# Kernel tuning notes

Measured on AMD Instinct MI355X. Metric: run time of the kernel, lower is better.

## Reference

```python
import jax, jax.numpy as jnp
import numpy as np

EMBED_DIM = 768
N_HEADS = 12
HEAD_DIM = EMBED_DIM // N_HEADS
B, T = 2, 4096


def setup_inputs() -> dict:
    key = jax.random.key(0)
    k1, k2, k3, k4, k5 = jax.random.split(key, 5)
    s = 1.0 / np.sqrt(EMBED_DIM)
    return {
        "x": jax.random.normal(k1, (B, T, EMBED_DIM), dtype=jnp.float32),
        "Wqkv": jax.random.normal(k2, (EMBED_DIM, 3 * EMBED_DIM), dtype=jnp.float32) * s,
        "bqkv": jnp.zeros((3 * EMBED_DIM,), dtype=jnp.float32),
        "Wproj": jax.random.normal(k3, (EMBED_DIM, EMBED_DIM), dtype=jnp.float32) * s,
        "bproj": jnp.zeros((EMBED_DIM,), dtype=jnp.float32),
    }


def reference(x, Wqkv, bqkv, Wproj, bproj):
    Bz, Tz, C = x.shape
    qkv = x @ Wqkv + bqkv                         # [B,T,3C]
    q, k, v = jnp.split(qkv, 3, axis=2)
    # [B,T,H,D] -> [B,H,T,D]
    def heads(t):
        return t.reshape(Bz, Tz, N_HEADS, HEAD_DIM).transpose(0, 2, 1, 3)
    q, k, v = heads(q), heads(k), heads(v)
    scale = 1.0 / np.sqrt(HEAD_DIM)
    att = jnp.einsum("bhqd,bhkd->bhqk", q, k) * scale   # [B,H,T,T]
    causal = jnp.tril(jnp.ones((Tz, Tz), dtype=bool))
    att = jnp.where(causal[None, None], att, -jnp.inf)
    att = jax.nn.softmax(att, axis=-1)
    y = jnp.einsum("bhqk,bhkd->bhqd", att, v)            # [B,H,T,D]
    y = y.transpose(0, 2, 1, 3).reshape(Bz, Tz, C)
    return y @ Wproj + bproj
```

## Files before the change

kernel.cpp:

```cpp
#include <hip/hip_runtime.h>
#include <math.h>
#include <stdint.h>

typedef __attribute__((ext_vector_type(8))) short bf16x8;
typedef __attribute__((ext_vector_type(4))) float f32x4;

__device__ __forceinline__ unsigned short f2bf(float f) {
    union { float f; unsigned u; } v; v.f = f;
    return (unsigned short)((v.u + 0x7fffu + ((v.u >> 16) & 1u)) >> 16);
}

__device__ __forceinline__ void gld_lds16(const void* g, void* l) {
    __builtin_amdgcn_global_load_lds(
        (const __attribute__((address_space(1))) unsigned*)(uintptr_t)g,
        (__attribute__((address_space(3))) unsigned*)(uintptr_t)l, 16, 0, 0);
}

__global__ void k_convert(const float* __restrict__ in, unsigned short* __restrict__ out, int n4) {
    int i = blockIdx.x * blockDim.x + threadIdx.x;
    if (i >= n4) return;
    float4 f = ((const float4*)in)[i];
    ushort4 o;
    o.x = f2bf(f.x); o.y = f2bf(f.y); o.z = f2bf(f.z); o.w = f2bf(f.w);
    ((ushort4*)out)[i] = o;
}

__global__ void k_transpose(const float* __restrict__ in, unsigned short* __restrict__ out, int R, int C) {
    __shared__ float tile[32][33];
    int c0 = blockIdx.x * 32, r0 = blockIdx.y * 32;
    int tx = threadIdx.x, ty = threadIdx.y;
#pragma unroll
    for (int i = 0; i < 4; ++i)
        tile[ty + i * 8][tx] = in[(size_t)(r0 + ty + i * 8) * C + c0 + tx];
    __syncthreads();
#pragma unroll
    for (int i = 0; i < 4; ++i)
        out[(size_t)(c0 + ty + i * 8) * R + r0 + tx] = f2bf(tile[tx][ty + i * 8]);
}

#define LDT 32

__device__ __forceinline__ void gemm_core(
    const unsigned short* __restrict__ A, const unsigned short* __restrict__ Bt,
    int K, unsigned short* As, unsigned short* Bs, f32x4 (&acc)[4][4])
{
    const int tid  = threadIdx.x;
    const int lane = tid & 63;
    const int w    = tid >> 6;
    const int wm   = (w >> 1) * 64, wn = (w & 1) * 64;
    const int l15  = lane & 15, quad = lane >> 4;
    const int m0 = blockIdx.x * 128, n0 = blockIdx.y * 128;

    const f32x4 zero = {0.f, 0.f, 0.f, 0.f};
#pragma unroll
    for (int i = 0; i < 4; ++i)
#pragma unroll
        for (int j = 0; j < 4; ++j) acc[i][j] = zero;

    const int r0 = tid >> 2, p8 = (tid & 3) * 8;
    const unsigned short* Ag0 = A  + (size_t)(m0 + r0) * K + p8;
    const unsigned short* Ag1 = A  + (size_t)(m0 + r0 + 64) * K + p8;
    const unsigned short* Bg0 = Bt + (size_t)(n0 + r0) * K + p8;
    const unsigned short* Bg1 = Bt + (size_t)(n0 + r0 + 64) * K + p8;
    unsigned short* lA0 = As + r0 * LDT + p8;
    unsigned short* lA1 = lA0 + 64 * LDT;
    unsigned short* lB0 = Bs + r0 * LDT + p8;
    unsigned short* lB1 = lB0 + 64 * LDT;

    const int nk = K >> 5;
    for (int kt = 0; kt < nk; ++kt) {
        __syncthreads();
        gld_lds16(Ag0, lA0);
        gld_lds16(Ag1, lA1);
        gld_lds16(Bg0, lB0);
        gld_lds16(Bg1, lB1);
        Ag0 += 32; Ag1 += 32; Bg0 += 32; Bg1 += 32;
        __syncthreads();
        bf16x8 af[4], bfr[4];
#pragma unroll
        for (int mi = 0; mi < 4; ++mi)
            af[mi] = *(const bf16x8*)&As[(wm + mi * 16 + l15) * LDT + quad * 8];
#pragma unroll
        for (int nj = 0; nj < 4; ++nj)
            bfr[nj] = *(const bf16x8*)&Bs[(wn + nj * 16 + l15) * LDT + quad * 8];
#pragma unroll
        for (int mi = 0; mi < 4; ++mi)
#pragma unroll
            for (int nj = 0; nj < 4; ++nj)
                acc[mi][nj] = __builtin_amdgcn_mfma_f32_16x16x32_bf16(af[mi], bfr[nj], acc[mi][nj], 0, 0, 0);
    }
}

__global__ __launch_bounds__(256) void k_gemm_qkv(
    const unsigned short* __restrict__ A, const unsigned short* __restrict__ Bt,
    const float* __restrict__ bias,
    unsigned short* __restrict__ QL, unsigned short* __restrict__ KL,
    unsigned short* __restrict__ VL)
{
    __shared__ __align__(16) unsigned short As[128 * LDT];
    __shared__ __align__(16) unsigned short Bs[128 * LDT];
    f32x4 acc[4][4];
    gemm_core(A, Bt, 768, As, Bs, acc);

    const int tid = threadIdx.x, lane = tid & 63, w = tid >> 6;
    const int wm = (w >> 1) * 64, wn = (w & 1) * 64;
    const int l15 = lane & 15, quad = lane >> 4;
    const int m0 = blockIdx.x * 128, n0 = blockIdx.y * 128;
    const float cscale = 0.18033688011f;
#pragma unroll
    for (int nj = 0; nj < 4; ++nj) {
        int cg = n0 + wn + nj * 16 + l15;
        float bv = bias[cg];
        int which = cg / 768;
        int rem = cg - which * 768;
        int hd = rem >> 6, d = rem & 63;
        float sc = (which == 0) ? cscale : 1.0f;
#pragma unroll
        for (int mi = 0; mi < 4; ++mi) {
#pragma unroll
            for (int r = 0; r < 4; ++r) {
                int rg = m0 + wm + mi * 16 + quad * 4 + r;
                int b = rg >> 12, tk = rg & 4095;
                int bh = b * 12 + hd;
                unsigned short ob = f2bf((acc[mi][nj][r] + bv) * sc);
                if (which == 0) {
                    size_t idx = ((((size_t)bh * 128 + (tk >> 5)) * 2 + ((tk >> 4) & 1)) * 2 + (d >> 5)) * 512
                               + ((d >> 3) & 3) * 128 + (tk & 15) * 8 + (d & 7);
                    QL[idx] = ob;
                } else if (which == 1) {
                    size_t idx = ((((size_t)bh * 64 + (tk >> 6)) * 4 + ((tk >> 4) & 3)) * 2 + (d >> 5)) * 512
                               + ((d >> 3) & 3) * 128 + (tk & 15) * 8 + (d & 7);
                    KL[idx] = ob;
                } else {
                    int wi = tk & 63;
                    size_t idx = ((((size_t)bh * 64 + (tk >> 6)) * 4 + (d >> 4)) * 2 + (wi >> 5)) * 512
                               + ((wi >> 3) & 3) * 128 + (d & 15) * 8 + (wi & 7);
                    VL[idx] = ob;
                }
            }
        }
    }
}

__global__ __launch_bounds__(256) void k_gemm_proj(
    const unsigned short* __restrict__ A, const unsigned short* __restrict__ Bt,
    const float* __restrict__ bias, float* __restrict__ out)
{
    __shared__ __align__(16) unsigned short As[128 * LDT];
    __shared__ __align__(16) unsigned short Bs[128 * LDT];
    f32x4 acc[4][4];
    gemm_core(A, Bt, 768, As, Bs, acc);

    const int tid = threadIdx.x, lane = tid & 63, w = tid >> 6;
    const int wm = (w >> 1) * 64, wn = (w & 1) * 64;
    const int l15 = lane & 15, quad = lane >> 4;
    const int m0 = blockIdx.x * 128, n0 = blockIdx.y * 128;
#pragma unroll
    for (int nj = 0; nj < 4; ++nj) {
        int cg = n0 + wn + nj * 16 + l15;
        float bv = bias[cg];
#pragma unroll
        for (int mi = 0; mi < 4; ++mi)
#pragma unroll
            for (int r = 0; r < 4; ++r) {
                int rg = m0 + wm + mi * 16 + quad * 4 + r;
                out[(size_t)rg * 768 + cg] = acc[mi][nj][r] + bv;
            }
    }
}

#define LDP 68

__global__ __launch_bounds__(256) void k_attn(
    const unsigned short* __restrict__ QL, const unsigned short* __restrict__ KL,
    const unsigned short* __restrict__ VL, unsigned short* __restrict__ Y)
{
    __shared__ __align__(16) char smem[34816];
    unsigned short* Ps = (unsigned short*)smem;
    float* Cb = (float*)smem;

    const int tid = threadIdx.x, lane = tid & 63;
    const int w = __builtin_amdgcn_readfirstlane(tid >> 6);
    const int l15 = lane & 15, quad = lane >> 4;
    const int id = blockIdx.x;
    const int bh = id % 24;
    const int qi = 127 - id / 24;
    const int q0 = qi * 32;
    const int nkt = qi / 2 + 1;
    const int lo = (nkt * w) >> 2, hi = (nkt * (w + 1)) >> 2;
    unsigned short* Pw = Ps + w * 2 * 32 * LDP;

    const int pw_off = l15 * LDP + quad * 4;
    const int pr_off = l15 * LDP + quad * 8;

    const unsigned short* Qb = QL + (((size_t)bh * 128 + qi) * 4) * 512 + lane * 8;
    const unsigned short* kp = KL + ((size_t)bh * 64 + lo) * 4096 + lane * 8;
    const unsigned short* vp = VL + ((size_t)bh * 64 + lo) * 4096 + lane * 8;

    bf16x8 qt[2][2];
#pragma unroll
    for (int m = 0; m < 2; ++m)
#pragma unroll
        for (int h = 0; h < 2; ++h)
            qt[m][h] = *(const bf16x8*)(Qb + (m * 2 + h) * 512);

    const f32x4 zero = {0.f, 0.f, 0.f, 0.f};
    f32x4 O[2][4], lac[2];
#pragma unroll
    for (int m = 0; m < 2; ++m) {
        lac[m] = zero;
#pragma unroll
        for (int dj = 0; dj < 4; ++dj) O[m][dj] = zero;
    }

    const short ONE = (short)0x3F80;
    const bf16x8 onesf = {ONE, ONE, ONE, ONE, ONE, ONE, ONE, ONE};

    if (lo < hi) {
        bf16x8 ka[4][2], vf[4][2];
#pragma unroll
        for (int i = 0; i < 4; ++i)
#pragma unroll
            for (int h = 0; h < 2; ++h)
                ka[i][h] = *(const bf16x8*)(kp + (i * 2 + h) * 512);
#pragma unroll
        for (int dj = 0; dj < 4; ++dj)
#pragma unroll
            for (int h = 0; h < 2; ++h)
                vf[dj][h] = *(const bf16x8*)(vp + (dj * 2 + h) * 512);

        {
            f32x4 st[2][4];
#pragma unroll
            for (int i = 0; i < 4; ++i)
#pragma unroll
                for (int m = 0; m < 2; ++m) {
                    f32x4 z = __builtin_amdgcn_mfma_f32_16x16x32_bf16(ka[i][0], qt[m][0], zero, 0, 0, 0);
                    st[m][i] = __builtin_amdgcn_mfma_f32_16x16x32_bf16(ka[i][1], qt[m][1], z, 0, 0, 0);
                }
            if (lo == nkt - 1) {
                const int kb = lo * 64;
#pragma unroll
                for (int m = 0; m < 2; ++m)
#pragma unroll
                    for (int i = 0; i < 4; ++i)
#pragma unroll
                        for (int r = 0; r < 4; ++r)
                            if (kb + i * 16 + quad * 4 + r > q0 + m * 16 + l15)
                                st[m][i][r] = -INFINITY;
            }
#pragma unroll
            for (int m = 0; m < 2; ++m)
#pragma unroll
                for (int i = 0; i < 4; ++i) {
                    unsigned e0 = __float_as_uint(__builtin_amdgcn_exp2f(st[m][i][0])) + 0x8000u;
                    unsigned e1 = __float_as_uint(__builtin_amdgcn_exp2f(st[m][i][1])) + 0x8000u;
                    unsigned e2 = __float_as_uint(__builtin_amdgcn_exp2f(st[m][i][2])) + 0x8000u;
                    unsigned e3 = __float_as_uint(__builtin_amdgcn_exp2f(st[m][i][3])) + 0x8000u;
                    uint2 pk;
                    pk.x = __builtin_amdgcn_perm(e1, e0, 0x07060302);
                    pk.y = __builtin_amdgcn_perm(e3, e2, 0x07060302);
                    *(uint2*)(Pw + pw_off + m * 16 * LDP + i * 16) = pk;
                }
        }

        for (int kt = lo; kt < hi; ++kt) {
            unsigned short* bc = Pw + ((kt - lo) & 1) * 32 * LDP;
            unsigned short* bn = Pw + (((kt - lo) & 1) ^ 1) * 32 * LDP;
            const bool more = (kt + 1 < hi);

            bf16x8 pa[2][2];
#pragma unroll
            for (int m = 0; m < 2; ++m) {
                pa[m][0] = *(const bf16x8*)(bc + pr_off + m * 16 * LDP);
                pa[m][1] = *(const bf16x8*)(bc + pr_off + m * 16 * LDP + 32);
            }

            if (more) {
                kp += 4096;
#pragma unroll
                for (int i = 0; i < 4; ++i)
#pragma unroll
                    for (int h = 0; h < 2; ++h)
                        ka[i][h] = *(const bf16x8*)(kp + (i * 2 + h) * 512);
            }

#pragma unroll
            for (int m = 0; m < 2; ++m) {
                f32x4 z = __builtin_amdgcn_mfma_f32_16x16x32_bf16(pa[m][0], onesf, lac[m], 0, 0, 0);
                lac[m] = __builtin_amdgcn_mfma_f32_16x16x32_bf16(pa[m][1], onesf, z, 0, 0, 0);
            }
#pragma unroll
            for (int dj = 0; dj < 4; ++dj)
#pragma unroll
                for (int m = 0; m < 2; ++m) {
                    f32x4 z = __builtin_amdgcn_mfma_f32_16x16x32_bf16(pa[m][0], vf[dj][0], O[m][dj], 0, 0, 0);
                    O[m][dj] = __builtin_amdgcn_mfma_f32_16x16x32_bf16(pa[m][1], vf[dj][1], z, 0, 0, 0);
                }

            if (more) {
                vp += 4096;
#pragma unroll
                for (int dj = 0; dj < 4; ++dj)
#pragma unroll
                    for (int h = 0; h < 2; ++h)
                        vf[dj][h] = *(const bf16x8*)(vp + (dj * 2 + h) * 512);

                f32x4 st[2][4];
#pragma unroll
                for (int i = 0; i < 4; ++i)
#pragma unroll
                    for (int m = 0; m < 2; ++m) {
                        f32x4 z = __builtin_amdgcn_mfma_f32_16x16x32_bf16(ka[i][0], qt[m][0], zero, 0, 0, 0);
                        st[m][i] = __builtin_amdgcn_mfma_f32_16x16x32_bf16(ka[i][1], qt[m][1], z, 0, 0, 0);
                    }
                if (kt + 1 == nkt - 1) {
                    const int kb = (kt + 1) * 64;
#pragma unroll
                    for (int m = 0; m < 2; ++m)
#pragma unroll
                        for (int i = 0; i < 4; ++i)
#pragma unroll
                            for (int r = 0; r < 4; ++r)
                                if (kb + i * 16 + quad * 4 + r > q0 + m * 16 + l15)
                                    st[m][i][r] = -INFINITY;
                }
#pragma unroll
                for (int m = 0; m < 2; ++m)
#pragma unroll
                    for (int i = 0; i < 4; ++i) {
                        unsigned e0 = __float_as_uint(__builtin_amdgcn_exp2f(st[m][i][0])) + 0x8000u;
                        unsigned e1 = __float_as_uint(__builtin_amdgcn_exp2f(st[m][i][1])) + 0x8000u;
                        unsigned e2 = __float_as_uint(__builtin_amdgcn_exp2f(st[m][i][2])) + 0x8000u;
                        unsigned e3 = __float_as_uint(__builtin_amdgcn_exp2f(st[m][i][3])) + 0x8000u;
                        uint2 pk;
                        pk.x = __builtin_amdgcn_perm(e1, e0, 0x07060302);
                        pk.y = __builtin_amdgcn_perm(e3, e2, 0x07060302);
                        *(uint2*)(bn + pw_off + m * 16 * LDP + i * 16) = pk;
                    }
            }
        }
    }

    __syncthreads();
    if (w > 0) {
        float* Ow = Cb + (w - 1) * 2560;
#pragma unroll
        for (int m = 0; m < 2; ++m) {
#pragma unroll
            for (int dj = 0; dj < 4; ++dj)
                *(f32x4*)&Ow[(m * 4 + dj) * 256 + lane * 4] = O[m][dj];
            *(f32x4*)&Ow[2048 + m * 256 + lane * 4] = lac[m];
        }
    }
    __syncthreads();
    if (w == 0) {
#pragma unroll
        for (int c = 0; c < 3; ++c) {
            const float* Ow = Cb + c * 2560;
#pragma unroll
            for (int m = 0; m < 2; ++m) {
#pragma unroll
                for (int dj = 0; dj < 4; ++dj)
                    O[m][dj] += *(const f32x4*)&Ow[(m * 4 + dj) * 256 + lane * 4];
                lac[m] += *(const f32x4*)&Ow[2048 + m * 256 + lane * 4];
            }
        }
        const int b = bh / 12, hd = bh % 12;
#pragma unroll
        for (int m = 0; m < 2; ++m)
#pragma unroll
            for (int r = 0; r < 4; ++r) {
                float inv = 1.0f / lac[m][r];
                int t = q0 + 16 * m + quad * 4 + r;
                size_t base = ((size_t)(b * 4096 + t)) * 768 + hd * 64;
#pragma unroll
                for (int dj = 0; dj < 4; ++dj)
                    Y[base + dj * 16 + l15] = f2bf(O[m][dj][r] * inv);
            }
    }
}

extern "C" void kernel_launch(void* const* d_in, const int* in_sizes, int n_in,
                              void* d_out, int out_size, void* d_ws, size_t ws_size,
                              hipStream_t stream) {
    (void)in_sizes; (void)n_in; (void)out_size; (void)ws_size;
    const float* x     = (const float*)d_in[0];
    const float* Wqkv  = (const float*)d_in[1];
    const float* bqkv  = (const float*)d_in[2];
    const float* Wproj = (const float*)d_in[3];
    const float* bproj = (const float*)d_in[4];
    float* out = (float*)d_out;

    char* ws = (char*)d_ws;
    size_t off = 0;
    auto alloc = [&](size_t bytes) -> void* {
        void* p = ws + off;
        off += (bytes + 255) & ~(size_t)255;
        return p;
    };
    unsigned short* xb     = (unsigned short*)alloc((size_t)8192 * 768 * 2);
    unsigned short* WqkvT  = (unsigned short*)alloc((size_t)2304 * 768 * 2);
    unsigned short* WprojT = (unsigned short*)alloc((size_t)768 * 768 * 2);
    unsigned short* QLb    = (unsigned short*)alloc((size_t)24 * 4096 * 64 * 2);
    unsigned short* KLb    = (unsigned short*)alloc((size_t)24 * 4096 * 64 * 2);
    unsigned short* VLb    = (unsigned short*)alloc((size_t)24 * 4096 * 64 * 2);
    unsigned short* Yb     = (unsigned short*)alloc((size_t)8192 * 768 * 2);

    k_convert<<<6144, 256, 0, stream>>>(x, xb, 8192 * 768 / 4);
    dim3 tb(32, 8);
    k_transpose<<<dim3(72, 24), tb, 0, stream>>>(Wqkv, WqkvT, 768, 2304);
    k_transpose<<<dim3(24, 24), tb, 0, stream>>>(Wproj, WprojT, 768, 768);
    k_gemm_qkv<<<dim3(64, 18), 256, 0, stream>>>(xb, WqkvT, bqkv, QLb, KLb, VLb);
    k_attn<<<dim3(3072), 256, 0, stream>>>(QLb, KLb, VLb, Yb);
    k_gemm_proj<<<dim3(64, 6), 256, 0, stream>>>(Yb, WprojT, bproj, out);
}
```

Baseline: 254.0 us.

## Assign one query tile per wave and balance blocks with a snake schedule

```diff
diff --git a/kernel.cpp b/kernel.cpp
--- a/kernel.cpp
+++ b/kernel.cpp
@@ -177,25 +177,27 @@
 {
     __shared__ __align__(16) char smem[34816];
     unsigned short* Ps = (unsigned short*)smem;
-    float* Cb = (float*)smem;
 
     const int tid = threadIdx.x, lane = tid & 63;
     const int w = __builtin_amdgcn_readfirstlane(tid >> 6);
     const int l15 = lane & 15, quad = lane >> 4;
     const int id = blockIdx.x;
     const int bh = id % 24;
-    const int qi = 127 - id / 24;
+    const int j = id / 24;
+    const int b3 = j / 11, a11 = j - b3 * 11;
+    const int g = (b3 == 0) ? a11 : (b3 == 1) ? (21 - a11) : (22 + a11);
+    const int qi = g * 4 + w;
     const int q0 = qi * 32;
-    const int nkt = qi / 2 + 1;
-    const int lo = (nkt * w) >> 2, hi = (nkt * (w + 1)) >> 2;
+    const int nkt = 2 * g + 2;
+    const int kmask = q0 >> 6;
     unsigned short* Pw = Ps + w * 2 * 32 * LDP;
 
     const int pw_off = l15 * LDP + quad * 4;
     const int pr_off = l15 * LDP + quad * 8;
 
     const unsigned short* Qb = QL + (((size_t)bh * 128 + qi) * 4) * 512 + lane * 8;
-    const unsigned short* kp = KL + ((size_t)bh * 64 + lo) * 4096 + lane * 8;
-    const unsigned short* vp = VL + ((size_t)bh * 64 + lo) * 4096 + lane * 8;
+    const unsigned short* kp = KL + ((size_t)bh * 64) * 4096 + lane * 8;
+    const unsigned short* vp = VL + ((size_t)bh * 64) * 4096 + lane * 8;
 
     bf16x8 qt[2][2];
 #pragma unroll
@@ -216,20 +218,96 @@
     const short ONE = (short)0x3F80;
     const bf16x8 onesf = {ONE, ONE, ONE, ONE, ONE, ONE, ONE, ONE};
 
-    if (lo < hi) {
-        bf16x8 ka[4][2], vf[4][2];
+    bf16x8 ka[4][2], vf[4][2];
+#pragma unroll
+    for (int i = 0; i < 4; ++i)
+#pragma unroll
+        for (int h = 0; h < 2; ++h)
+            ka[i][h] = *(const bf16x8*)(kp + (i * 2 + h) * 512);
+#pragma unroll
+    for (int dj = 0; dj < 4; ++dj)
+#pragma unroll
+        for (int h = 0; h < 2; ++h)
+            vf[dj][h] = *(const bf16x8*)(vp + (dj * 2 + h) * 512);
+
+    {
+        f32x4 st[2][4];
 #pragma unroll
         for (int i = 0; i < 4; ++i)
 #pragma unroll
-            for (int h = 0; h < 2; ++h)
-                ka[i][h] = *(const bf16x8*)(kp + (i * 2 + h) * 512);
+            for (int m = 0; m < 2; ++m) {
+                f32x4 z = __builtin_amdgcn_mfma_f32_16x16x32_bf16(ka[i][0], qt[m][0], zero, 0, 0, 0);
+                st[m][i] = __builtin_amdgcn_mfma_f32_16x16x32_bf16(ka[i][1], qt[m][1], z, 0, 0, 0);
+            }
+        if (kmask == 0) {
+#pragma unroll
+            for (int m = 0; m < 2; ++m)
+#pragma unroll
+                for (int i = 0; i < 4; ++i)
+#pragma unroll
+                    for (int r = 0; r < 4; ++r)
+                        if (i * 16 + quad * 4 + r > q0 + m * 16 + l15)
+                            st[m][i][r] = -INFINITY;
+        }
+#pragma unroll
+        for (int m = 0; m < 2; ++m)
+#pragma unroll
+            for (int i = 0; i < 4; ++i) {
+                unsigned e0 = __float_as_uint(__builtin_amdgcn_exp2f(st[m][i][0])) + 0x8000u;
+                unsigned e1 = __float_as_uint(__builtin_amdgcn_exp2f(st[m][i][1])) + 0x8000u;
+                unsigned e2 = __float_as_uint(__builtin_amdgcn_exp2f(st[m][i][2])) + 0x8000u;
+                unsigned e3 = __float_as_uint(__builtin_amdgcn_exp2f(st[m][i][3])) + 0x8000u;
+                uint2 pk;
+                pk.x = __builtin_amdgcn_perm(e1, e0, 0x07060302);
+                pk.y = __builtin_amdgcn_perm(e3, e2, 0x07060302);
+                *(uint2*)(Pw + pw_off + m * 16 * LDP + i * 16) = pk;
+            }
+    }
+
+    for (int kt = 0; kt < nkt; ++kt) {
+        __builtin_amdgcn_s_barrier();
+
+        unsigned short* bc = Pw + (kt & 1) * 32 * LDP;
+        unsigned short* bn = Pw + ((kt & 1) ^ 1) * 32 * LDP;
+        const bool more = (kt + 1 < nkt);
+
+        bf16x8 pa[2][2];
+#pragma unroll
+        for (int m = 0; m < 2; ++m) {
+            pa[m][0] = *(const bf16x8*)(bc + pr_off + m * 16 * LDP);
+            pa[m][1] = *(const bf16x8*)(bc + pr_off + m * 16 * LDP + 32);
+        }
+
+        if (more) {
+            kp += 4096;
+#pragma unroll
+            for (int i = 0; i < 4; ++i)
+#pragma unroll
+                for (int h = 0; h < 2; ++h)
+                    ka[i][h] = *(const bf16x8*)(kp + (i * 2 + h) * 512);
+        }
+
+#pragma unroll
+        for (int m = 0; m < 2; ++m) {
+            f32x4 z = __builtin_amdgcn_mfma_f32_16x16x32_bf16(pa[m][0], onesf, lac[m], 0, 0, 0);
+            lac[m] = __builtin_amdgcn_mfma_f32_16x16x32_bf16(pa[m][1], onesf, z, 0, 0, 0);
+        }
 #pragma unroll
         for (int dj = 0; dj < 4; ++dj)
 #pragma unroll
-            for (int h = 0; h < 2; ++h)
-                vf[dj][h] = *(const bf16x8*)(vp + (dj * 2 + h) * 512);
-
-        {
+            for (int m = 0; m < 2; ++m) {
+                f32x4 z = __builtin_amdgcn_mfma_f32_16x16x32_bf16(pa[m][0], vf[dj][0], O[m][dj], 0, 0, 0);
+                O[m][dj] = __builtin_amdgcn_mfma_f32_16x16x32_bf16(pa[m][1], vf[dj][1], z, 0, 0, 0);
+            }
+
+        if (more) {
+            vp += 4096;
+#pragma unroll
+            for (int dj = 0; dj < 4; ++dj)
+#pragma unroll
+                for (int h = 0; h < 2; ++h)
+                    vf[dj][h] = *(const bf16x8*)(vp + (dj * 2 + h) * 512);
+
             f32x4 st[2][4];
 #pragma unroll
             for (int i = 0; i < 4; ++i)
@@ -238,8 +316,8 @@
                     f32x4 z = __builtin_amdgcn_mfma_f32_16x16x32_bf16(ka[i][0], qt[m][0], zero, 0, 0, 0);
                     st[m][i] = __builtin_amdgcn_mfma_f32_16x16x32_bf16(ka[i][1], qt[m][1], z, 0, 0, 0);
                 }
-            if (lo == nkt - 1) {
-                const int kb = lo * 64;
+            if (kt + 1 >= kmask) {
+                const int kb = (kt + 1) * 64;
 #pragma unroll
                 for (int m = 0; m < 2; ++m)
 #pragma unroll
@@ -260,125 +338,23 @@
                     uint2 pk;
                     pk.x = __builtin_amdgcn_perm(e1, e0, 0x07060302);
                     pk.y = __builtin_amdgcn_perm(e3, e2, 0x07060302);
-                    *(uint2*)(Pw + pw_off + m * 16 * LDP + i * 16) = pk;
+                    *(uint2*)(bn + pw_off + m * 16 * LDP + i * 16) = pk;
                 }
         }
-
-        for (int kt = lo; kt < hi; ++kt) {
-            unsigned short* bc = Pw + ((kt - lo) & 1) * 32 * LDP;
-            unsigned short* bn = Pw + (((kt - lo) & 1) ^ 1) * 32 * LDP;
-            const bool more = (kt + 1 < hi);
-
-            bf16x8 pa[2][2];
-#pragma unroll
-            for (int m = 0; m < 2; ++m) {
-                pa[m][0] = *(const bf16x8*)(bc + pr_off + m * 16 * LDP);
-                pa[m][1] = *(const bf16x8*)(bc + pr_off + m * 16 * LDP + 32);
-            }
-
-            if (more) {
-                kp += 4096;
-#pragma unroll
-                for (int i = 0; i < 4; ++i)
-#pragma unroll
-                    for (int h = 0; h < 2; ++h)
-                        ka[i][h] = *(const bf16x8*)(kp + (i * 2 + h) * 512);
-            }
-
-#pragma unroll
-            for (int m = 0; m < 2; ++m) {
-                f32x4 z = __builtin_amdgcn_mfma_f32_16x16x32_bf16(pa[m][0], onesf, lac[m], 0, 0, 0);
-                lac[m] = __builtin_amdgcn_mfma_f32_16x16x32_bf16(pa[m][1], onesf, z, 0, 0, 0);
-            }
+    }
+
+    const int b = bh / 12, hd = bh % 12;
+#pragma unroll
+    for (int m = 0; m < 2; ++m)
+#pragma unroll
+        for (int r = 0; r < 4; ++r) {
+            float inv = 1.0f / lac[m][r];
+            int t = q0 + 16 * m + quad * 4 + r;
+            size_t base = ((size_t)(b * 4096 + t)) * 768 + hd * 64;
 #pragma unroll
             for (int dj = 0; dj < 4; ++dj)
-#pragma unroll
-                for (int m = 0; m < 2; ++m) {
-                    f32x4 z = __builtin_amdgcn_mfma_f32_16x16x32_bf16(pa[m][0], vf[dj][0], O[m][dj], 0, 0, 0);
-                    O[m][dj] = __builtin_amdgcn_mfma_f32_16x16x32_bf16(pa[m][1], vf[dj][1], z, 0, 0, 0);
-                }
-
-            if (more) {
-                vp += 4096;
-#pragma unroll
-                for (int dj = 0; dj < 4; ++dj)
-#pragma unroll
-                    for (int h = 0; h < 2; ++h)
-                        vf[dj][h] = *(const bf16x8*)(vp + (dj * 2 + h) * 512);
-
-                f32x4 st[2][4];
-#pragma unroll
-                for (int i = 0; i < 4; ++i)
-#pragma unroll
-                    for (int m = 0; m < 2; ++m) {
-                        f32x4 z = __builtin_amdgcn_mfma_f32_16x16x32_bf16(ka[i][0], qt[m][0], zero, 0, 0, 0);
-                        st[m][i] = __builtin_amdgcn_mfma_f32_16x16x32_bf16(ka[i][1], qt[m][1], z, 0, 0, 0);
-                    }
-                if (kt + 1 == nkt - 1) {
-                    const int kb = (kt + 1) * 64;
-#pragma unroll
-                    for (int m = 0; m < 2; ++m)
-#pragma unroll
-                        for (int i = 0; i < 4; ++i)
-#pragma unroll
-                            for (int r = 0; r < 4; ++r)
-                                if (kb + i * 16 + quad * 4 + r > q0 + m * 16 + l15)
-                                    st[m][i][r] = -INFINITY;
-                }
-#pragma unroll
-                for (int m = 0; m < 2; ++m)
-#pragma unroll
-                    for (int i = 0; i < 4; ++i) {
-                        unsigned e0 = __float_as_uint(__builtin_amdgcn_exp2f(st[m][i][0])) + 0x8000u;
-                        unsigned e1 = __float_as_uint(__builtin_amdgcn_exp2f(st[m][i][1])) + 0x8000u;
-                        unsigned e2 = __float_as_uint(__builtin_amdgcn_exp2f(st[m][i][2])) + 0x8000u;
-                        unsigned e3 = __float_as_uint(__builtin_amdgcn_exp2f(st[m][i][3])) + 0x8000u;
-                        uint2 pk;
-                        pk.x = __builtin_amdgcn_perm(e1, e0, 0x07060302);
-                        pk.y = __builtin_amdgcn_perm(e3, e2, 0x07060302);
-                        *(uint2*)(bn + pw_off + m * 16 * LDP + i * 16) = pk;
-                    }
-            }
-        }
-    }
-
-    __syncthreads();
-    if (w > 0) {
-        float* Ow = Cb + (w - 1) * 2560;
-#pragma unroll
-        for (int m = 0; m < 2; ++m) {
-#pragma unroll
-            for (int dj = 0; dj < 4; ++dj)
-                *(f32x4*)&Ow[(m * 4 + dj) * 256 + lane * 4] = O[m][dj];
-            *(f32x4*)&Ow[2048 + m * 256 + lane * 4] = lac[m];
-        }
-    }
-    __syncthreads();
-    if (w == 0) {
-#pragma unroll
-        for (int c = 0; c < 3; ++c) {
-            const float* Ow = Cb + c * 2560;
-#pragma unroll
-            for (int m = 0; m < 2; ++m) {
-#pragma unroll
-                for (int dj = 0; dj < 4; ++dj)
-                    O[m][dj] += *(const f32x4*)&Ow[(m * 4 + dj) * 256 + lane * 4];
-                lac[m] += *(const f32x4*)&Ow[2048 + m * 256 + lane * 4];
-            }
-        }
-        const int b = bh / 12, hd = bh % 12;
-#pragma unroll
-        for (int m = 0; m < 2; ++m)
-#pragma unroll
-            for (int r = 0; r < 4; ++r) {
-                float inv = 1.0f / lac[m][r];
-                int t = q0 + 16 * m + quad * 4 + r;
-                size_t base = ((size_t)(b * 4096 + t)) * 768 + hd * 64;
-#pragma unroll
-                for (int dj = 0; dj < 4; ++dj)
-                    Y[base + dj * 16 + l15] = f2bf(O[m][dj][r] * inv);
-            }
-    }
+                Y[base + dj * 16 + l15] = f2bf(O[m][dj][r] * inv);
+        }
 }
 
 extern "C" void kernel_launch(void* const* d_in, const int* in_sizes, int n_in,
@@ -412,6 +388,6 @@
     k_transpose<<<dim3(72, 24), tb, 0, stream>>>(Wqkv, WqkvT, 768, 2304);
     k_transpose<<<dim3(24, 24), tb, 0, stream>>>(Wproj, WprojT, 768, 768);
     k_gemm_qkv<<<dim3(64, 18), 256, 0, stream>>>(xb, WqkvT, bqkv, QLb, KLb, VLb);
-    k_attn<<<dim3(3072), 256, 0, stream>>>(QLb, KLb, VLb, Yb);
+    k_attn<<<dim3(768), 256, 0, stream>>>(QLb, KLb, VLb, Yb);
     k_gemm_proj<<<dim3(64, 6), 256, 0, stream>>>(Yb, WprojT, bproj, out);
 }
```

After: 291.5 us. 1.15x slower.
